# Kernel optimization log

Hardware: AMD Instinct MI355X
Metric: run time of the kernel (lower is better)

## Reference

```python
import jax, jax.numpy as jnp
import numpy as np
import math

B, C, H, W = 8, 512, 32, 32
ENC = 1024
L2 = 64
NH = 8
GROUPS = 32
EPS = 1e-5

def group_norm(x, gamma, beta):
    # x: (B, C, L) GroupNorm with 32 groups (float32)
    b, c, l = x.shape
    xg = x.reshape(b, GROUPS, (c // GROUPS) * l)
    mean = xg.mean(-1, keepdims=True)
    var = xg.var(-1, keepdims=True)
    xn = ((xg - mean) * jax.lax.rsqrt(var + EPS)).reshape(b, c, l)
    return xn * gamma[None, :, None] + beta[None, :, None]

def conv1x1(w, bias, x):
    # conv_nd(1, in, out, 1): w (out, in), x (B, in, L) -> (B, out, L)
    return jnp.einsum('oc,bcl->bol', w, x) + bias[None, :, None]

def setup_inputs() -> dict:
    key = jax.random.key(0)
    ks = jax.random.split(key, 16)
    s = lambda fan_in: 1.0 / math.sqrt(fan_in)
    inp = {
        'x': jax.random.normal(ks[0], (B, C, H, W), jnp.float32),
        'xf_out': jax.random.normal(ks[1], (B, ENC, L2), jnp.float32),
        'obj_class_embedding': jax.random.normal(ks[2], (B, ENC, L2), jnp.float32),
        'obj_bbox_embedding': jax.random.normal(ks[3], (B, ENC, L2), jnp.float32),
        'image_patch_bbox_embedding': jax.random.normal(ks[4], (B, ENC, H * W), jnp.float32),
        'key_padding_mask': jax.random.bernoulli(ks[5], 0.3, (B, L2)),
        'qkv_w': jax.random.normal(ks[6], (3 * C, C), jnp.float32) * s(C),
        'qkv_b': jnp.zeros((3 * C,), jnp.float32),
        'g_qkv': jnp.ones((C,), jnp.float32),
        'b_qkv': jnp.zeros((C,), jnp.float32),
        'lc_w': jax.random.normal(ks[7], (2 * C, ENC), jnp.float32) * s(ENC),
        'lc_b': jnp.zeros((2 * C,), jnp.float32),
        'lp_w': jax.random.normal(ks[8], (C, ENC), jnp.float32) * s(ENC),
        'lp_b': jnp.zeros((C,), jnp.float32),
        'g_obj': jnp.ones((ENC,), jnp.float32),
        'b_obj': jnp.zeros((ENC,), jnp.float32),
        'g_lpos': jnp.ones((C,), jnp.float32),
        'b_lpos': jnp.zeros((C,), jnp.float32),
        'g_ipos': jnp.ones((C,), jnp.float32),
        'b_ipos': jnp.zeros((C,), jnp.float32),
        # proj_out is zero-initialized in the original (zero_module); use random
        # weights so the projection math is exercised non-trivially.
        'proj_w': jax.random.normal(ks[9], (C, C), jnp.float32) * s(C),
        'proj_b': jnp.zeros((C,), jnp.float32),
    }
    return inp

def reference(x, xf_out, obj_class_embedding, obj_bbox_embedding,
              image_patch_bbox_embedding, key_padding_mask,
              qkv_w, qkv_b, g_qkv, b_qkv, lc_w, lc_b, lp_w, lp_b,
              g_obj, b_obj, g_lpos, b_lpos, g_ipos, b_ipos, proj_w, proj_b):
    b, c, h, w = x.shape
    L1 = h * w
    d = C // NH
    xf = x.reshape(b, c, L1)

    qkv = conv1x1(qkv_w, qkv_b, group_norm(xf, g_qkv, b_qkv))  # (B, 3C, L1)
    q, k, v = jnp.split(qkv, 3, axis=1)
    q = q.reshape(b * NH, d, L1)
    k = k.reshape(b * NH, d, L1)
    v = v.reshape(b * NH, d, L1)

    ipp = group_norm(conv1x1(lp_w, lp_b, image_patch_bbox_embedding), g_ipos, b_ipos)
    ipp = ipp.reshape(b * NH, d, L1)

    q_img = jnp.concatenate([q, ipp], axis=1)  # (B*H, 2d, L1)
    k_img = jnp.concatenate([k, ipp], axis=1)

    lpe = group_norm(conv1x1(lp_w, lp_b, obj_bbox_embedding), g_lpos, b_lpos)
    lpe = lpe.reshape(b * NH, d, L2)

    lce = (xf_out + group_norm(obj_class_embedding, g_obj, b_obj)) / 2
    kl, vl = jnp.split(conv1x1(lc_w, lc_b, lce), 2, axis=1)
    kl = kl.reshape(b * NH, d, L2)
    vl = vl.reshape(b * NH, d, L2)
    k_layout = jnp.concatenate([kl, lpe], axis=1)  # (B*H, 2d, L2)

    k_mix = jnp.concatenate([k_img, k_layout], axis=2)  # (B*H, 2d, L1+L2)
    v_mix = jnp.concatenate([v, vl], axis=2)             # (B*H, d, L1+L2)

    mask = jnp.concatenate([jnp.zeros((b, L1), bool), key_padding_mask], axis=1)  # (B, L1+L2)

    scale = 1.0 / math.sqrt(math.sqrt(2 * C // NH))
    attn = jnp.einsum('bct,bcs->bts', q_img * scale, k_mix * scale)  # (B*H, L1, L1+L2)
    attn = attn.reshape(b, NH, L1, L1 + L2)
    attn = jnp.where(mask[:, None, None, :], -jnp.inf, attn)
    attn = jax.nn.softmax(attn.astype(jnp.float32), axis=-1).astype(attn.dtype)
    attn = attn.reshape(b * NH, L1, L1 + L2)

    out = jnp.einsum('bts,bcs->bct', attn, v_mix).reshape(b, C, L1)
    hproj = conv1x1(proj_w, proj_b, out)
    return (xf + hproj).reshape(b, c, h, w)
```

## Files before the change

kernel.cpp:

```cpp
#include <hip/hip_runtime.h>
#include <math.h>

#define NB 8
#define NC 512
#define NL1 1024
#define NL2 64
#define NLKV 1088
#define NENC 1024
#define EPSV 1e-5f
#define SCALE2 0.08838834764831845f
#define SCALE2Q 0.12752425f
#define DEFER_THR 11.5415603f

typedef _Float16 half8 __attribute__((ext_vector_type(8)));
typedef _Float16 half4 __attribute__((ext_vector_type(4)));
typedef __fp16 fp16x2 __attribute__((ext_vector_type(2)));
typedef float f32x4 __attribute__((ext_vector_type(4)));
typedef float f32x16 __attribute__((ext_vector_type(16)));
typedef unsigned int uint32x2 __attribute__((ext_vector_type(2)));

__device__ __forceinline__ void gload16(const _Float16* g, _Float16* l) {
  __builtin_amdgcn_global_load_lds(
      (const __attribute__((address_space(1))) void*)g,
      (__attribute__((address_space(3))) void*)l, 16, 0, 0);
}

__device__ __forceinline__ unsigned int pkrtz(float a, float b) {
  union { fp16x2 hh; unsigned int uu; } cv;
  cv.hh = __builtin_amdgcn_cvt_pkrtz(a, b);
  return cv.uu;
}

__device__ __forceinline__ float fast_exp2(float x) {
  return __builtin_amdgcn_exp2f(x);
}

__global__ __launch_bounds__(256) void k_init(
    const float* __restrict__ x, const float* __restrict__ obj,
    float* __restrict__ xm, float* __restrict__ xr,
    float* __restrict__ om, float* __restrict__ orr,
    const float* __restrict__ qkv_w, _Float16* __restrict__ w16qkv,
    const float* __restrict__ lp_w, _Float16* __restrict__ w16lp,
    const float* __restrict__ proj_w, _Float16* __restrict__ w16proj,
    const float* __restrict__ lc_w, _Float16* __restrict__ w16lc)
{
  int bid = blockIdx.x;
  if (bid < 512) {
    const float* p; float* meanp; float* rstdp; int n4, n, bg;
    if (bid < 256) {
      bg = bid;
      int b = bg >> 5, g = bg & 31;
      p = x + ((size_t)b * 512 + (size_t)g * 16) * 1024;
      n = 16 * 1024; meanp = xm; rstdp = xr;
    } else {
      bg = bid - 256;
      int b = bg >> 5, g = bg & 31;
      p = obj + ((size_t)b * 1024 + (size_t)g * 32) * 64;
      n = 32 * 64; meanp = om; rstdp = orr;
    }
    n4 = n >> 2;
    float s = 0.f, s2 = 0.f;
    for (int i = threadIdx.x; i < n4; i += 256) {
      float4 v = ((const float4*)p)[i];
      s += v.x + v.y + v.z + v.w;
      s2 += v.x * v.x + v.y * v.y + v.z * v.z + v.w * v.w;
    }
    #pragma unroll
    for (int o = 32; o > 0; o >>= 1) { s += __shfl_down(s, o); s2 += __shfl_down(s2, o); }
    __shared__ float rs[4], rq[4];
    int lane = threadIdx.x & 63, w = threadIdx.x >> 6;
    if (lane == 0) { rs[w] = s; rq[w] = s2; }
    __syncthreads();
    if (threadIdx.x == 0) {
      float S = rs[0] + rs[1] + rs[2] + rs[3];
      float Q = rq[0] + rq[1] + rq[2] + rq[3];
      float m = S / n;
      float v = Q / n - m * m;
      if (v < 0.f) v = 0.f;
      meanp[bg] = m;
      rstdp[bg] = rsqrtf(v + EPSV);
    }
  } else {
    int cb = bid - 512;
    const float* s; _Float16* d; int i4;
    if (cb < 768)        { s = qkv_w;  d = w16qkv;  i4 = cb * 256 + threadIdx.x; }
    else if (cb < 1280)  { s = lp_w;   d = w16lp;   i4 = (cb - 768) * 256 + threadIdx.x; }
    else if (cb < 1536)  { s = proj_w; d = w16proj; i4 = (cb - 1280) * 256 + threadIdx.x; }
    else                 { s = lc_w;   d = w16lc;   i4 = (cb - 1536) * 256 + threadIdx.x; }
    float4 v = *(const float4*)&s[(size_t)i4 * 4];
    half4 o; o.x = (_Float16)v.x; o.y = (_Float16)v.y; o.z = (_Float16)v.z; o.w = (_Float16)v.w;
    *(half4*)&d[(size_t)i4 * 4] = o;
  }
}

__global__ __launch_bounds__(256) void k_prep(
    const float* __restrict__ x, const float* __restrict__ xm, const float* __restrict__ xr,
    const float* __restrict__ g_qkv, const float* __restrict__ b_qkv, _Float16* __restrict__ xT,
    const float* __restrict__ ipbe, _Float16* __restrict__ ipbeT,
    const float* __restrict__ xf_out, const float* __restrict__ obj_class,
    const float* __restrict__ obj_bbox,
    const float* __restrict__ om, const float* __restrict__ orr,
    const float* __restrict__ g_obj, const float* __restrict__ b_obj,
    _Float16* __restrict__ lceT, _Float16* __restrict__ objT)
{
  __shared__ _Float16 tile[64][72];
  const int bid = blockIdx.x;
  const int tl = threadIdx.x & 63;
  if (bid < 1024) {
    const int tt = bid & 15, ct = (bid >> 4) & 7, b = bid >> 7;
    const int c0 = ct * 64, t0 = tt * 64;
    const int cp = threadIdx.x >> 6;
    #pragma unroll
    for (int i = 0; i < 16; i++) {
      int c = c0 + i * 4 + cp;
      float v = x[((size_t)b * NC + c) * NL1 + t0 + tl];
      int g = c >> 4;
      float ga = g_qkv[c] * xr[b * 32 + g];
      float be = b_qkv[c] - xm[b * 32 + g] * ga;
      tile[tl][i * 4 + cp] = (_Float16)(v * ga + be);
    }
    __syncthreads();
    int tr = threadIdx.x >> 2, c16 = (threadIdx.x & 3) * 16;
    _Float16* dst = xT + ((size_t)b * 1024 + t0 + tr) * 512 + c0 + c16;
    *(half8*)dst = *(half8*)&tile[tr][c16];
    *(half8*)(dst + 8) = *(half8*)&tile[tr][c16 + 8];
  } else if (bid < 3072) {
    const int e2 = bid - 1024;
    const int tt = e2 & 15, et = (e2 >> 4) & 15, b = e2 >> 8;
    const int e0 = et * 64, t0 = tt * 64;
    const int ep = threadIdx.x >> 6;
    #pragma unroll
    for (int i = 0; i < 16; i++) {
      int e = e0 + i * 4 + ep;
      tile[tl][i * 4 + ep] = (_Float16)ipbe[((size_t)b * 1024 + e) * 1024 + t0 + tl];
    }
    __syncthreads();
    int tr = threadIdx.x >> 2, c16 = (threadIdx.x & 3) * 16;
    _Float16* d = ipbeT + ((size_t)b * 1024 + t0 + tr) * 1024 + e0 + c16;
    *(half8*)d = *(half8*)&tile[tr][c16];
    *(half8*)(d + 8) = *(half8*)&tile[tr][c16 + 8];
  } else {
    const int e2 = bid - 3072;
    const int et = e2 & 15, which = (e2 >> 4) & 1, b = e2 >> 5;
    const int e0 = et * 64;
    const int ep = threadIdx.x >> 6;
    if (which == 0) {
      #pragma unroll
      for (int i = 0; i < 16; i++) {
        int e = e0 + i * 4 + ep;
        size_t idx = ((size_t)b * 1024 + e) * 64 + tl;
        int g = e >> 5;
        float xn = (obj_class[idx] - om[b * 32 + g]) * orr[b * 32 + g] * g_obj[e] + b_obj[e];
        tile[tl][i * 4 + ep] = (_Float16)(0.5f * (xf_out[idx] + xn));
      }
    } else {
      #pragma unroll
      for (int i = 0; i < 16; i++) {
        int e = e0 + i * 4 + ep;
        tile[tl][i * 4 + ep] = (_Float16)obj_bbox[((size_t)b * 1024 + e) * 64 + tl];
      }
    }
    __syncthreads();
    int tr = threadIdx.x >> 2, c16 = (threadIdx.x & 3) * 16;
    _Float16* dst = (which == 0 ? lceT : objT) + ((size_t)b * 64 + tr) * 1024 + e0 + c16;
    *(half8*)dst = *(half8*)&tile[tr][c16];
    *(half8*)(dst + 8) = *(half8*)&tile[tr][c16 + 8];
  }
}

#define MFMA_CORE(KTOT)                                                                  \
  f32x4 acc[4][4];                                                                       \
  _Pragma("unroll") for (int i_ = 0; i_ < 4; i_++)                                       \
      _Pragma("unroll") for (int j_ = 0; j_ < 4; j_++) acc[i_][j_] = (f32x4)0.f;         \
  {                                                                                      \
    const int rsub = lane >> 3, csrc = (lane & 7) ^ rsub;                                \
    const int NT_ = (KTOT) / 64;                                                         \
    _Pragma("unroll") for (int i = 0; i < 4; i++) {                                      \
      int seg = w * 4 + i;                                                               \
      int row = seg * 8 + rsub;                                                          \
      gload16(Abase + (size_t)(m0 + row) * (KTOT) + csrc * 8, ldsA + seg * 512);         \
      gload16(Bbase + (size_t)(n0 + row) * (KTOT) + csrc * 8, ldsB + seg * 512);         \
    }                                                                                    \
    __syncthreads();                                                                     \
    int cur_ = 0;                                                                        \
    for (int t_ = 0; t_ < NT_; t_++) {                                                   \
      if (t_ + 1 < NT_) {                                                                \
        _Float16* da_ = ldsA + ((cur_ ^ 1) << 13);                                       \
        _Float16* db_ = ldsB + ((cur_ ^ 1) << 13);                                       \
        int kt = (t_ + 1) * 64;                                                          \
        _Pragma("unroll") for (int i = 0; i < 4; i++) {                                  \
          int seg = w * 4 + i;                                                           \
          int row = seg * 8 + rsub;                                                      \
          gload16(Abase + (size_t)(m0 + row) * (KTOT) + kt + csrc * 8, da_ + seg * 512); \
          gload16(Bbase + (size_t)(n0 + row) * (KTOT) + kt + csrc * 8, db_ + seg * 512); \
        }                                                                                \
      }                                                                                  \
      const char* ra_ = (const char*)(ldsA + (cur_ << 13));                              \
      const char* rb_ = (const char*)(ldsB + (cur_ << 13));                              \
      _Pragma("unroll") for (int kk = 0; kk < 2; kk++) {                                 \
        half8 af[4], bf[4];                                                              \
        _Pragma("unroll") for (int mb = 0; mb < 4; mb++) {                               \
          int row = wm + mb * 16 + l15;                                                  \
          af[mb] = *(const half8*)(ra_ + row * 128 +                                     \
                                   ((kk * 64 + lg * 16) ^ ((row & 7) << 4)));            \
        }                                                                                \
        _Pragma("unroll") for (int nb = 0; nb < 4; nb++) {                               \
          int row = wn + nb * 16 + l15;                                                  \
          bf[nb] = *(const half8*)(rb_ + row * 128 +                                     \
                                   ((kk * 64 + lg * 16) ^ ((row & 7) << 4)));            \
        }                                                                                \
        _Pragma("unroll") for (int mb = 0; mb < 4; mb++)                                 \
            _Pragma("unroll") for (int nb = 0; nb < 4; nb++)                             \
                acc[mb][nb] = __builtin_amdgcn_mfma_f32_16x16x32_f16(af[mb], bf[nb],     \
                                                                    acc[mb][nb], 0, 0, 0);\
      }                                                                                  \
      __syncthreads();                                                                   \
      cur_ ^= 1;                                                                         \
    }                                                                                    \
  }

#define MFMA_CORE_N64(KTOT)                                                              \
  f32x4 acc[4][2];                                                                       \
  _Pragma("unroll") for (int i_ = 0; i_ < 4; i_++)                                       \
      _Pragma("unroll") for (int j_ = 0; j_ < 2; j_++) acc[i_][j_] = (f32x4)0.f;         \
  {                                                                                      \
    const int rsub = lane >> 3, csrc = (lane & 7) ^ rsub;                                \
    const int NT_ = (KTOT) / 64;                                                         \
    _Pragma("unroll") for (int i = 0; i < 4; i++) {                                      \
      int seg = w * 4 + i;                                                               \
      int row = seg * 8 + rsub;                                                          \
      gload16(Abase + (size_t)(m0 + row) * (KTOT) + csrc * 8, ldsA + seg * 512);         \
    }                                                                                    \
    _Pragma("unroll") for (int i = 0; i < 2; i++) {                                      \
      int seg = w * 2 + i;                                                               \
      int row = seg * 8 + rsub;                                                          \
      gload16(Bbase + (size_t)row * (KTOT) + csrc * 8, ldsB + seg * 512);                \
    }                                                                                    \
    __syncthreads();                                                                     \
    int cur_ = 0;                                                                        \
    for (int t_ = 0; t_ < NT_; t_++) {                                                   \
      if (t_ + 1 < NT_) {                                                                \
        _Float16* da_ = ldsA + ((cur_ ^ 1) << 13);                                       \
        _Float16* db_ = ldsB + ((cur_ ^ 1) << 12);                                       \
        int kt = (t_ + 1) * 64;                                                          \
        _Pragma("unroll") for (int i = 0; i < 4; i++) {                                  \
          int seg = w * 4 + i;                                                           \
          int row = seg * 8 + rsub;                                                      \
          gload16(Abase + (size_t)(m0 + row) * (KTOT) + kt + csrc * 8, da_ + seg * 512); \
        }                                                                                \
        _Pragma("unroll") for (int i = 0; i < 2; i++) {                                  \
          int seg = w * 2 + i;                                                           \
          int row = seg * 8 + rsub;                                                      \
          gload16(Bbase + (size_t)row * (KTOT) + kt + csrc * 8, db_ + seg * 512);        \
        }                                                                                \
      }                                                                                  \
      const char* ra_ = (const char*)(ldsA + (cur_ << 13));                              \
      const char* rb_ = (const char*)(ldsB + (cur_ << 12));                              \
      _Pragma("unroll") for (int kk = 0; kk < 2; kk++) {                                 \
        half8 af[4], bf[2];                                                              \
        _Pragma("unroll") for (int mb = 0; mb < 4; mb++) {                               \
          int row = wm + mb * 16 + l15;                                                  \
          af[mb] = *(const half8*)(ra_ + row * 128 +                                     \
                                   ((kk * 64 + lg * 16) ^ ((row & 7) << 4)));            \
        }                                                                                \
        _Pragma("unroll") for (int nb = 0; nb < 2; nb++) {                               \
          int row = wn + nb * 16 + l15;                                                  \
          bf[nb] = *(const half8*)(rb_ + row * 128 +                                     \
                                   ((kk * 64 + lg * 16) ^ ((row & 7) << 4)));            \
        }                                                                                \
        _Pragma("unroll") for (int mb = 0; mb < 4; mb++)                                 \
            _Pragma("unroll") for (int nb = 0; nb < 2; nb++)                             \
                acc[mb][nb] = __builtin_amdgcn_mfma_f32_16x16x32_f16(af[mb], bf[nb],     \
                                                                    acc[mb][nb], 0, 0, 0);\
      }                                                                                  \
      __syncthreads();                                                                   \
      cur_ ^= 1;                                                                         \
    }                                                                                    \
  }

__global__ __launch_bounds__(256) void k_mfma_big(
    const _Float16* __restrict__ w16qkv, const float* __restrict__ qkv_b,
    const _Float16* __restrict__ xhatT,
    const _Float16* __restrict__ w16lp, const float* __restrict__ lp_b,
    const _Float16* __restrict__ ipbeT,
    const _Float16* __restrict__ w16lc, const float* __restrict__ lc_b,
    const _Float16* __restrict__ lceT, const _Float16* __restrict__ objT,
    const float* __restrict__ g_lpos, const float* __restrict__ b_lpos,
    _Float16* __restrict__ qT, _Float16* __restrict__ kT, _Float16* __restrict__ vT,
    _Float16* __restrict__ ipp16)
{
  __shared__ _Float16 smem[32768];
  const int bid0 = blockIdx.x;
  const int tid = threadIdx.x, lane = tid & 63, w = tid >> 6;
  const int l15 = lane & 15, lg = lane >> 4;

  if (bid0 < 256) {
    const int nt = bid0 & 7, mt = (bid0 >> 3) & 3, b = bid0 >> 5;
    const int m0 = mt * 128, n0 = nt * 128;
    _Float16* ldsA = smem;
    _Float16* ldsB = smem + 16384;
    const _Float16* Abase = w16lp;
    const _Float16* Bbase = ipbeT + (size_t)b * 1024 * 1024;
    const int wm = (w >> 1) * 64, wn = (w & 1) * 64;
    MFMA_CORE(1024)
    #pragma unroll
    for (int mb = 0; mb < 4; mb++) {
      #pragma unroll
      for (int r = 0; r < 4; r++) {
        int m = m0 + wm + mb * 16 + lg * 4 + r;
        float bia = lp_b[m];
        #pragma unroll
        for (int nb = 0; nb < 4; nb++) {
          int t = n0 + wn + nb * 16 + l15;
          ipp16[((size_t)b * NC + m) * NL1 + t] = (_Float16)(acc[mb][nb][r] + bia);
        }
      }
    }
  } else if (bid0 < 352) {
    const int local = bid0 - 256;
    const int mt = local % 12, b = local / 12;
    const bool islc = (mt < 8);
    const int m0 = (islc ? mt : mt - 8) * 128;
    _Float16* ldsA = smem;
    _Float16* ldsB = smem + 16384;
    float (*red_s)[4] = (float(*)[4])(smem + 24576);
    float (*red_q)[4] = (float(*)[4])(smem + 24608);
    const _Float16* Abase = islc ? w16lc : w16lp;
    const float* bias = islc ? lc_b : lp_b;
    const _Float16* Bbase = (islc ? lceT : objT) + (size_t)b * 64 * 1024;
    const int wm = (w >> 1) * 64, wn = (w & 1) * 32;
    MFMA_CORE_N64(1024)

    if (islc) {
      #pragma unroll
      for (int mb = 0; mb < 4; mb++) {
        #pragma unroll
        for (int r = 0; r < 4; r++) {
          int m = m0 + wm + mb * 16 + lg * 4 + r;
          float bia = bias[m];
          #pragma unroll
          for (int nb = 0; nb < 2; nb++) {
            int l = wn + nb * 16 + l15;
            float val = acc[mb][nb][r] + bia;
            if (m < 512) {
              int h = m >> 6, dc = m & 63;
              kT[(((size_t)b * 8 + h) * 1088 + 1024 + l) * 128 + dc] = (_Float16)val;
            } else {
              int mv = m - 512, h = mv >> 6, dc = mv & 63;
              vT[(((size_t)b * 8 + h) * 64 + dc) * 1088 + 1024 + l] = (_Float16)val;
            }
          }
        }
      }
    } else {
      float vals[4][2][4];
      float ps[4], pq[4];
      #pragma unroll
      for (int mb = 0; mb < 4; mb++) {
        ps[mb] = 0.f; pq[mb] = 0.f;
        #pragma unroll
        for (int r = 0; r < 4; r++) {
          int m = m0 + wm + mb * 16 + lg * 4 + r;
          float bia = bias[m];
          #pragma unroll
          for (int nb = 0; nb < 2; nb++) {
            float val = acc[mb][nb][r] + bia;
            vals[mb][nb][r] = val;
            ps[mb] += val; pq[mb] += val * val;
          }
        }
      }
      #pragma unroll
      for (int mb = 0; mb < 4; mb++) {
        #pragma unroll
        for (int o = 32; o > 0; o >>= 1) {
          ps[mb] += __shfl_xor(ps[mb], o);
          pq[mb] += __shfl_xor(pq[mb], o);
        }
      }
      if (lane == 0) {
        #pragma unroll
        for (int mb = 0; mb < 4; mb++) { red_s[w][mb] = ps[mb]; red_q[w][mb] = pq[mb]; }
      }
      __syncthreads();
      const int wbase = (wm >> 6) * 2;
      #pragma unroll
      for (int mb = 0; mb < 4; mb++) {
        float S = red_s[wbase][mb] + red_s[wbase + 1][mb];
        float Q = red_q[wbase][mb] + red_q[wbase + 1][mb];
        float mean = S * (1.f / 1024.f);
        float var = Q * (1.f / 1024.f) - mean * mean;
        if (var < 0.f) var = 0.f;
        float rstd = rsqrtf(var + EPSV);
        #pragma unroll
        for (int r = 0; r < 4; r++) {
          int c = m0 + wm + mb * 16 + lg * 4 + r;
          float ga = g_lpos[c] * rstd;
          float be = b_lpos[c] - mean * ga;
          int hh = c >> 6, dc = c & 63;
          #pragma unroll
          for (int nb = 0; nb < 2; nb++) {
            int l = wn + nb * 16 + l15;
            float xn = vals[mb][nb][r] * ga + be;
            kT[(((size_t)b * 8 + hh) * 1088 + 1024 + l) * 128 + 64 + dc] = (_Float16)xn;
          }
        }
      }
    }
  } else {
    const int bid = bid0 - 352;
    const int nt = bid & 7, tt = bid >> 3;
    const int mt = tt % 12, b = tt / 12;
    const int m0 = mt * 128, n0 = nt * 128;
    _Float16* ldsA = smem;
    _Float16* ldsB = smem + 16384;
    const _Float16* Abase = w16qkv;
    const _Float16* Bbase = xhatT + (size_t)b * 1024 * 512;
    const int wm = (w >> 1) * 64, wn = (w & 1) * 64;
    MFMA_CORE(512)

    char* tb = (char*)smem;
    if (m0 < 1024) {
      const bool isq = (m0 < 512);
      const float qs = isq ? SCALE2Q : 1.f;
      #pragma unroll
      for (int mb = 0; mb < 4; mb++) {
        #pragma unroll
        for (int r = 0; r < 4; r++) {
          int mcol = wm + mb * 16 + lg * 4 + r;
          float bia = qkv_b[m0 + mcol];
          #pragma unroll
          for (int nb = 0; nb < 4; nb++) {
            int trow = wn + nb * 16 + l15;
            float val = (acc[mb][nb][r] + bia) * qs;
            *(_Float16*)(tb + ((trow * 256 + mcol * 2) ^ ((trow & 7) << 4))) = (_Float16)val;
          }
        }
      }
      __syncthreads();
      #pragma unroll
      for (int it = 0; it < 8; it++) {
        int e = it * 256 + tid;
        int trow = e >> 4, seg = e & 15;
        half8 v = *(const half8*)(tb + ((trow * 256 + seg * 16) ^ ((trow & 7) << 4)));
        if (isq) {
          int mq = m0 + seg * 8, hh = mq >> 6, dc = mq & 63;
          *(half8*)(qT + (((size_t)b * 8 + hh) * 1024 + n0 + trow) * 128 + dc) = v;
        } else {
          int mk = m0 - 512 + seg * 8, hh = mk >> 6, dc = mk & 63;
          *(half8*)(kT + (((size_t)b * 8 + hh) * 1088 + n0 + trow) * 128 + dc) = v;
        }
      }
    } else {
      #pragma unroll
      for (int mb = 0; mb < 4; mb++) {
        #pragma unroll
        for (int r = 0; r < 4; r++) {
          int mrow = wm + mb * 16 + lg * 4 + r;
          float bia = qkv_b[m0 + mrow];
          #pragma unroll
          for (int nb = 0; nb < 4; nb++) {
            int tcol = wn + nb * 16 + l15;
            *(_Float16*)(tb + ((mrow * 256 + tcol * 2) ^ ((mrow & 7) << 4))) =
                (_Float16)(acc[mb][nb][r] + bia);
          }
        }
      }
      __syncthreads();
      #pragma unroll
      for (int it = 0; it < 8; it++) {
        int e = it * 256 + tid;
        int mrow = e >> 4, seg = e & 15;
        half8 v = *(const half8*)(tb + ((mrow * 256 + seg * 16) ^ ((mrow & 7) << 4)));
        int mv = m0 - 1024 + mrow, hh = mv >> 6, dc = mv & 63;
        *(half8*)(vT + (((size_t)b * 8 + hh) * 64 + dc) * 1088 + n0 + seg * 8) = v;
      }
    }
  }
}

__global__ __launch_bounds__(256) void k_mfma_proj(
    const _Float16* __restrict__ Abase, const float* __restrict__ bias,
    const _Float16* __restrict__ Ball, const float* __restrict__ xin,
    float* __restrict__ out)
{
  __shared__ _Float16 smem[24576];
  _Float16* ldsA = smem;
  _Float16* ldsB = smem + 16384;
  const int b = blockIdx.z, mt = blockIdx.y, nt = blockIdx.x;
  const int m0 = mt * 128, n0 = nt * 64;
  const _Float16* Bbase = Ball + (size_t)b * 1024 * 512 + (size_t)n0 * 512;
  const int tid = threadIdx.x, lane = tid & 63, w = tid >> 6;
  const int l15 = lane & 15, lg = lane >> 4;
  const int wm = (w >> 1) * 64, wn = (w & 1) * 32;
  MFMA_CORE_N64(512)
  #pragma unroll
  for (int mb = 0; mb < 4; mb++) {
    #pragma unroll
    for (int r = 0; r < 4; r++) {
      int m = m0 + wm + mb * 16 + lg * 4 + r;
      float bia = bias[m];
      #pragma unroll
      for (int nb = 0; nb < 2; nb++) {
        int t = n0 + wn + nb * 16 + l15;
        size_t idx = ((size_t)b * NC + m) * NL1 + t;
        out[idx] = xin[idx] + acc[mb][nb][r] + bia;
      }
    }
  }
}

__global__ __launch_bounds__(256) void k_ipp_fuse(
    const _Float16* __restrict__ raw,
    const float* __restrict__ gm, const float* __restrict__ gb,
    _Float16* __restrict__ qT, _Float16* __restrict__ kT)
{
  const int g = blockIdx.x, b = blockIdx.y;
  const int tid = threadIdx.x;
  const _Float16* p = raw + ((size_t)b * 512 + (size_t)g * 16) * 1024;
  const int t0 = tid * 4;

  float4 v[16];
  float s = 0.f, s2 = 0.f;
  #pragma unroll
  for (int c = 0; c < 16; c++) {
    half4 hv = *(const half4*)&p[(size_t)c * 1024 + t0];
    v[c].x = (float)hv.x; v[c].y = (float)hv.y; v[c].z = (float)hv.z; v[c].w = (float)hv.w;
    s += v[c].x + v[c].y + v[c].z + v[c].w;
    s2 += v[c].x * v[c].x + v[c].y * v[c].y + v[c].z * v[c].z + v[c].w * v[c].w;
  }
  #pragma unroll
  for (int o = 32; o > 0; o >>= 1) { s += __shfl_down(s, o); s2 += __shfl_down(s2, o); }
  __shared__ float rs[4], rq[4], stat[2];
  int lane = tid & 63, w = tid >> 6;
  if (lane == 0) { rs[w] = s; rq[w] = s2; }
  __syncthreads();
  if (tid == 0) {
    float S = rs[0] + rs[1] + rs[2] + rs[3];
    float Q = rq[0] + rq[1] + rq[2] + rq[3];
    float mn = S / 16384.f;
    float var = Q / 16384.f - mn * mn;
    if (var < 0.f) var = 0.f;
    stat[0] = mn; stat[1] = rsqrtf(var + EPSV);
  }
  __syncthreads();
  const float mn = stat[0], rstd = stat[1];

  float ga[16], be[16];
  #pragma unroll
  for (int c = 0; c < 16; c++) {
    ga[c] = gm[g * 16 + c] * rstd;
    be[c] = gb[g * 16 + c] - mn * ga[c];
  }

  const size_t bh = (size_t)b * 8 + (g >> 2);
  const int dcb = (g & 3) * 16;
  #pragma unroll
  for (int j = 0; j < 4; j++) {
    const int t = t0 + j;
    half8 k0, k1, q0, q1;
    #pragma unroll
    for (int c = 0; c < 8; c++) {
      float4 vc = v[c];
      float e = (j == 0) ? vc.x : (j == 1) ? vc.y : (j == 2) ? vc.z : vc.w;
      float xn = e * ga[c] + be[c];
      k0[c] = (_Float16)xn;
      q0[c] = (_Float16)(SCALE2Q * xn);
    }
    #pragma unroll
    for (int c = 8; c < 16; c++) {
      float4 vc = v[c];
      float e = (j == 0) ? vc.x : (j == 1) ? vc.y : (j == 2) ? vc.z : vc.w;
      float xn = e * ga[c] + be[c];
      k1[c - 8] = (_Float16)xn;
      q1[c - 8] = (_Float16)(SCALE2Q * xn);
    }
    _Float16* qd = qT + (bh * 1024 + t) * 128 + 64 + dcb;
    _Float16* kd = kT + (bh * 1088 + t) * 128 + 64 + dcb;
    *(half8*)qd = q0; *(half8*)(qd + 8) = q1;
    *(half8*)kd = k0; *(half8*)(kd + 8) = k1;
  }
}

__global__ __launch_bounds__(256, 2) void k_attn_mfma(
    const _Float16* __restrict__ qT, const _Float16* __restrict__ kT,
    const _Float16* __restrict__ vT, const int* __restrict__ mask,
    _Float16* __restrict__ attnT)
{
  const int x = blockIdx.x & 7;
  const int k = blockIdx.x >> 3;
  const int bh = x + ((k >> 3) << 3);
  const int qt = k & 7;
  const int b = bh >> 3, h = bh & 7;
  const int tid = threadIdx.x;
  const int lane = tid & 63;
  const int w = tid >> 6;
  const int l31 = lane & 31;
  const int hi = lane >> 5;

  __shared__ _Float16 KsB[3 * 64 * 128];
  __shared__ _Float16 VtB[4 * 64 * 64];

  const int q = qt * 128 + w * 32 + l31;

  half8 aq[8];
  {
    const _Float16* qp = qT + ((size_t)bh * 1024 + q) * 128 + hi * 8;
    #pragma unroll
    for (int kst = 0; kst < 8; kst++) aq[kst] = *(const half8*)(qp + kst * 16);
  }

  unsigned int mbits = 0;
  {
    const int* mp = mask + b * 64;
    #pragma unroll
    for (int sb = 0; sb < 2; sb++) {
      #pragma unroll
      for (int reg = 0; reg < 16; reg++) {
        int s = sb * 32 + (reg & 3) + 8 * (reg >> 2) + 4 * hi;
        if (mp[s]) mbits |= 1u << (sb * 16 + reg);
      }
    }
  }

  f32x16 O0 = (f32x16)0.f, O1 = (f32x16)0.f;
  f32x16 scA0 = (f32x16)0.f, scA1 = (f32x16)0.f;
  f32x16 scB0 = (f32x16)0.f, scB1 = (f32x16)0.f;
  float m_run = -INFINITY, l_run = 0.f;

  const int kxor = (l31 & 7) << 4;
  const int ksrow_off = lane >> 4;
  const int kcsrc_base = lane & 15;
  const int vdc_off = lane >> 3;
  const int vcsrc_base = lane & 7;

#define STAGE_KV(T, KD, VD)                                                          \
  {                                                                                  \
    const int s0_ = (T) * 64;                                                        \
    _Pragma("unroll") for (int r = 0; r < 4; r++) {                                  \
      int seg = r * 4 + w;                                                           \
      int srow = seg * 4 + ksrow_off;                                                \
      int csrc = kcsrc_base ^ (srow & 7);                                            \
      gload16(kT + ((size_t)bh * 1088 + s0_ + srow) * 128 + csrc * 8, (KD) + seg * 512); \
    }                                                                                \
    _Pragma("unroll") for (int r = 0; r < 2; r++) {                                  \
      int seg = r * 4 + w;                                                           \
      int dc = seg * 8 + vdc_off;                                                    \
      int csrc = vcsrc_base ^ (dc & 7);                                              \
      gload16(vT + ((size_t)bh * 64 + dc) * 1088 + s0_ + csrc * 8, (VD) + seg * 512);  \
    }                                                                                \
  }

#define XHALF_FMAX(OUTV, INV)                                                        \
  { unsigned int xi_ = __float_as_uint(INV);                                         \
    uint32x2 xr_ = __builtin_amdgcn_permlane32_swap(xi_, xi_, false, false);         \
    OUTV = fmaxf(__uint_as_float(xr_.x), __uint_as_float(xr_.y)); }
#define XHALF_ADD(OUTV, INV)                                                         \
  { unsigned int xi_ = __float_as_uint(INV);                                         \
    uint32x2 xr_ = __builtin_amdgcn_permlane32_swap(xi_, xi_, false, false);         \
    OUTV = __uint_as_float(xr_.x) + __uint_as_float(xr_.y); }

#define ATTN_ITER(C0, C1, P0, P1, T)                                                 \
  {                                                                                  \
    const int T_ = (T);                                                              \
    if (T_ <= 16) {                                                                  \
      if (T_ <= 14) {                                                                \
        _Float16* kd_ = KsB + ((T_ + 2) % 3) * 8192;                                 \
        _Float16* vd_ = VtB + ((T_ + 2) & 3) * 4096;                                 \
        STAGE_KV(T_ + 2, kd_, vd_)                                                   \
      }                                                                              \
      const char* ksb_ = (const char*)(KsB + (T_ % 3) * 8192);                       \
      C0 = (f32x16)0.f; C1 = (f32x16)0.f;                                            \
      __builtin_amdgcn_s_setprio(1);                                                 \
      _Pragma("unroll") for (int kst = 0; kst < 8; kst++) {                          \
        half8 kf0 = *(const half8*)(ksb_ + ((l31 * 256 + kst * 32 + hi * 16) ^ kxor)); \
        half8 kf1 = *(const half8*)(ksb_ + (((32 + l31) * 256 + kst * 32 + hi * 16) ^ kxor)); \
        C0 = __builtin_amdgcn_mfma_f32_32x32x16_f16(kf0, aq[kst], C0, 0, 0, 0);      \
        C1 = __builtin_amdgcn_mfma_f32_32x32x16_f16(kf1, aq[kst], C1, 0, 0, 0);      \
      }                                                                              \
      __builtin_amdgcn_s_setprio(0);                                                 \
    }                                                                                \
    if (T_ >= 1) {                                                                   \
      if (T_ == 17) {                                                                \
        _Pragma("unroll") for (int i = 0; i < 16; i++) {                             \
          if ((mbits >> i) & 1)        P0[i] = -INFINITY;                            \
          if ((mbits >> (16 + i)) & 1) P1[i] = -INFINITY;                            \
        }                                                                            \
      }                                                                              \
      float mx;                                                                      \
      {                                                                              \
        float a0 = fmaxf(fmaxf(P0[0], P0[1]), P0[2]);                                \
        float a1 = fmaxf(fmaxf(P0[3], P0[4]), P0[5]);                                \
        float a2 = fmaxf(fmaxf(P0[6], P0[7]), P0[8]);                                \
        float a3 = fmaxf(fmaxf(P0[9], P0[10]), P0[11]);                              \
        float a4 = fmaxf(fmaxf(P0[12], P0[13]), P0[14]);                             \
        float a5 = fmaxf(fmaxf(P0[15], P1[0]), P1[1]);                               \
        float a6 = fmaxf(fmaxf(P1[2], P1[3]), P1[4]);                                \
        float a7 = fmaxf(fmaxf(P1[5], P1[6]), P1[7]);                                \
        float a8 = fmaxf(fmaxf(P1[8], P1[9]), P1[10]);                               \
        float a9 = fmaxf(fmaxf(P1[11], P1[12]), P1[13]);                             \
        float aa = fmaxf(P1[14], P1[15]);                                            \
        float b0 = fmaxf(fmaxf(a0, a1), a2);                                         \
        float b1 = fmaxf(fmaxf(a3, a4), a5);                                         \
        float b2 = fmaxf(fmaxf(a6, a7), a8);                                         \
        float b3 = fmaxf(a9, aa);                                                    \
        mx = fmaxf(fmaxf(b0, b1), fmaxf(b2, b3));                                    \
      }                                                                              \
      XHALF_FMAX(mx, mx)                                                             \
      if (__all(mx <= m_run + DEFER_THR)) {                                          \
        float sum = 0.f;                                                             \
        _Pragma("unroll") for (int i = 0; i < 16; i++) {                             \
          float p = fast_exp2(P0[i] - m_run); P0[i] = p; sum += p; }                 \
        _Pragma("unroll") for (int i = 0; i < 16; i++) {                             \
          float p = fast_exp2(P1[i] - m_run); P1[i] = p; sum += p; }                 \
        XHALF_ADD(sum, sum)                                                          \
        l_run += sum;                                                                \
      } else {                                                                       \
        float m_new = fmaxf(m_run, mx);                                              \
        float alpha = fast_exp2(m_run - m_new);                                      \
        float sum = 0.f;                                                             \
        _Pragma("unroll") for (int i = 0; i < 16; i++) {                             \
          float p = fast_exp2(P0[i] - m_new); P0[i] = p; sum += p; }                 \
        _Pragma("unroll") for (int i = 0; i < 16; i++) {                             \
          float p = fast_exp2(P1[i] - m_new); P1[i] = p; sum += p; }                 \
        XHALF_ADD(sum, sum)                                                          \
        l_run = l_run * alpha + sum;                                                 \
        m_run = m_new;                                                               \
        _Pragma("unroll") for (int i = 0; i < 16; i++) { O0[i] *= alpha; O1[i] *= alpha; } \
      }                                                                              \
      const char* vtb_ = (const char*)(VtB + ((T_ - 1) & 3) * 4096);                 \
      __builtin_amdgcn_s_setprio(1);                                                 \
      _Pragma("unroll") for (int sb = 0; sb < 2; sb++) {                             \
        _Pragma("unroll") for (int k2 = 0; k2 < 2; k2++) {                           \
          const int kst = sb * 2 + k2;                                               \
          unsigned int pa0, pa1, pb0, pb1;                                           \
          if (sb == 0) {                                                             \
            pa0 = pkrtz(P0[8 * k2 + 0], P0[8 * k2 + 1]);                             \
            pa1 = pkrtz(P0[8 * k2 + 2], P0[8 * k2 + 3]);                             \
            pb0 = pkrtz(P0[8 * k2 + 4], P0[8 * k2 + 5]);                             \
            pb1 = pkrtz(P0[8 * k2 + 6], P0[8 * k2 + 7]);                             \
          } else {                                                                   \
            pa0 = pkrtz(P1[8 * k2 + 0], P1[8 * k2 + 1]);                             \
            pa1 = pkrtz(P1[8 * k2 + 2], P1[8 * k2 + 3]);                             \
            pb0 = pkrtz(P1[8 * k2 + 4], P1[8 * k2 + 5]);                             \
            pb1 = pkrtz(P1[8 * k2 + 6], P1[8 * k2 + 7]);                             \
          }                                                                          \
          uint32x2 r0_ = __builtin_amdgcn_permlane32_swap(pa0, pb0, false, false);   \
          uint32x2 r1_ = __builtin_amdgcn_permlane32_swap(pa1, pb1, false, false);   \
          union { unsigned int u[4]; half8 hh; } pf;                                 \
          pf.u[0] = r0_.x;                                                           \
          pf.u[1] = r1_.x;                                                           \
          pf.u[2] = r0_.y;                                                           \
          pf.u[3] = r1_.y;                                                           \
          half8 vf0 = *(const half8*)(vtb_ + ((l31 * 128 + kst * 32 + hi * 16) ^ kxor)); \
          half8 vf1 = *(const half8*)(vtb_ + (((32 + l31) * 128 + kst * 32 + hi * 16) ^ kxor)); \
          O0 = __builtin_amdgcn_mfma_f32_32x32x16_f16(vf0, pf.hh, O0, 0, 0, 0);      \
          O1 = __builtin_amdgcn_mfma_f32_32x32x16_f16(vf1, pf.hh, O1, 0, 0, 0);      \
        }                                                                            \
      }                                                                              \
      __builtin_amdgcn_s_setprio(0);                                                 \
    }                                                                                \
    if (T_ < 17) {                                                                   \
      if (T_ <= 14)      asm volatile("s_waitcnt vmcnt(8)" ::: "memory");            \
      else if (T_ == 15) asm volatile("s_waitcnt vmcnt(2)" ::: "memory");            \
      else               asm volatile("s_waitcnt vmcnt(0)" ::: "memory");            \
      __builtin_amdgcn_s_barrier();                                                  \
    }                                                                                \
  }

  STAGE_KV(0, KsB, VtB)
  STAGE_KV(1, KsB + 8192, VtB + 4096)
  asm volatile("s_waitcnt vmcnt(8)" ::: "memory");
  __builtin_amdgcn_s_barrier();

  for (int t = 0; t < 18; t += 2) {
    ATTN_ITER(scA0, scA1, scB0, scB1, t)
    ATTN_ITER(scB0, scB1, scA0, scA1, t + 1)
  }

  float inv = 1.f / l_run;
  _Float16* op = attnT + ((size_t)b * 1024 + q) * 512 + h * 64;
  #pragma unroll
  for (int i = 0; i < 16; i += 2) {
    int dc = (i & 3) + 8 * (i >> 2) + 4 * hi;
    unsigned int c0 = pkrtz(O0[i] * inv, O0[i + 1] * inv);
    unsigned int c1 = pkrtz(O1[i] * inv, O1[i + 1] * inv);
    *(unsigned int*)(op + dc) = c0;
    *(unsigned int*)(op + 32 + dc) = c1;
  }
}

extern "C" void kernel_launch(void* const* d_in, const int* in_sizes, int n_in,
                              void* d_out, int out_size, void* d_ws, size_t ws_size,
                              hipStream_t stream) {
  const float* x         = (const float*)d_in[0];
  const float* xf_out    = (const float*)d_in[1];
  const float* obj_class = (const float*)d_in[2];
  const float* obj_bbox  = (const float*)d_in[3];
  const float* ipbe      = (const float*)d_in[4];
  const int*   mask      = (const int*)d_in[5];
  const float* qkv_w     = (const float*)d_in[6];
  const float* qkv_b     = (const float*)d_in[7];
  const float* g_qkv     = (const float*)d_in[8];
  const float* b_qkv     = (const float*)d_in[9];
  const float* lc_w      = (const float*)d_in[10];
  const float* lc_b      = (const float*)d_in[11];
  const float* lp_w      = (const float*)d_in[12];
  const float* lp_b      = (const float*)d_in[13];
  const float* g_obj     = (const float*)d_in[14];
  const float* b_obj     = (const float*)d_in[15];
  const float* g_lpos    = (const float*)d_in[16];
  const float* b_lpos    = (const float*)d_in[17];
  const float* g_ipos    = (const float*)d_in[18];
  const float* b_ipos    = (const float*)d_in[19];
  const float* proj_w    = (const float*)d_in[20];
  const float* proj_b    = (const float*)d_in[21];
  float* out = (float*)d_out;

  _Float16* f16b = (_Float16*)d_ws;
  _Float16* qT      = f16b;
  _Float16* kT      = qT + 8388608;
  _Float16* vT      = kT + 8912896;
  _Float16* xhatT   = vT + 4456448;
  _Float16* ipbeT   = xhatT + 4194304;
  _Float16* attnT   = ipbeT + 8388608;
  _Float16* w16qkv  = attnT + 4194304;
  _Float16* w16lp   = w16qkv + 786432;
  _Float16* w16proj = w16lp + 524288;
  _Float16* w16lc   = w16proj + 262144;
  _Float16* lceT    = w16lc + 1048576;
  _Float16* objT    = lceT + 524288;
  _Float16* ipp16   = objT + 524288;
  float* st = (float*)(ipp16 + 4194304);
  float* xm = st, * xr = st + 256, * om = st + 512, * orr = st + 768;

  dim3 blk(256);
  k_init<<<dim3(3072), blk, 0, stream>>>(x, obj_class, xm, xr, om, orr,
                                         qkv_w, w16qkv, lp_w, w16lp, proj_w, w16proj, lc_w, w16lc);
  k_prep<<<dim3(3328), blk, 0, stream>>>(x, xm, xr, g_qkv, b_qkv, xhatT,
                                         ipbe, ipbeT,
                                         xf_out, obj_class, obj_bbox, om, orr, g_obj, b_obj,
                                         lceT, objT);
  k_mfma_big<<<dim3(1120), blk, 0, stream>>>(w16qkv, qkv_b, xhatT,
                                             w16lp, lp_b, ipbeT,
                                             w16lc, lc_b, lceT, objT,
                                             g_lpos, b_lpos,
                                             qT, kT, vT, ipp16);
  k_ipp_fuse<<<dim3(32, 8), blk, 0, stream>>>(ipp16, g_ipos, b_ipos, qT, kT);
  k_attn_mfma<<<dim3(512), blk, 0, stream>>>(qT, kT, vT, mask, attnT);
  k_mfma_proj<<<dim3(16, 4, 8), blk, 0, stream>>>(w16proj, proj_b, attnT, x, out);
}
```

Measured before the change: 125.0 us.

## Process two query tiles per wave in attention, halving grid and K/V loads

```diff
diff --git a/kernel.cpp b/kernel.cpp
--- a/kernel.cpp
+++ b/kernel.cpp
@@ -582,15 +582,14 @@
   }
 }
 
-__global__ __launch_bounds__(256, 2) void k_attn_mfma(
+__global__ __launch_bounds__(256, 1) void k_attn_mfma(
     const _Float16* __restrict__ qT, const _Float16* __restrict__ kT,
     const _Float16* __restrict__ vT, const int* __restrict__ mask,
     _Float16* __restrict__ attnT)
 {
-  const int x = blockIdx.x & 7;
-  const int k = blockIdx.x >> 3;
-  const int bh = x + ((k >> 3) << 3);
-  const int qt = k & 7;
+  const int bid = blockIdx.x;
+  const int bh = bid >> 2;
+  const int qt = bid & 3;
   const int b = bh >> 3, h = bh & 7;
   const int tid = threadIdx.x;
   const int lane = tid & 63;
@@ -599,15 +598,20 @@
   const int hi = lane >> 5;
 
   __shared__ _Float16 KsB[3 * 64 * 128];
-  __shared__ _Float16 VtB[4 * 64 * 64];
-
-  const int q = qt * 128 + w * 32 + l31;
-
-  half8 aq[8];
+  __shared__ _Float16 VtB[3 * 64 * 64];
+
+  const int qA = qt * 256 + w * 64 + l31;
+  const int qB = qA + 32;
+
+  half8 aqA[8], aqB[8];
   {
-    const _Float16* qp = qT + ((size_t)bh * 1024 + q) * 128 + hi * 8;
-    #pragma unroll
-    for (int kst = 0; kst < 8; kst++) aq[kst] = *(const half8*)(qp + kst * 16);
+    const _Float16* qpA = qT + ((size_t)bh * 1024 + qA) * 128 + hi * 8;
+    const _Float16* qpB = qT + ((size_t)bh * 1024 + qB) * 128 + hi * 8;
+    #pragma unroll
+    for (int kst = 0; kst < 8; kst++) {
+      aqA[kst] = *(const half8*)(qpA + kst * 16);
+      aqB[kst] = *(const half8*)(qpB + kst * 16);
+    }
   }
 
   unsigned int mbits = 0;
@@ -623,10 +627,10 @@
     }
   }
 
-  f32x16 O0 = (f32x16)0.f, O1 = (f32x16)0.f;
-  f32x16 scA0 = (f32x16)0.f, scA1 = (f32x16)0.f;
-  f32x16 scB0 = (f32x16)0.f, scB1 = (f32x16)0.f;
-  float m_run = -INFINITY, l_run = 0.f;
+  f32x16 OA0 = (f32x16)0.f, OA1 = (f32x16)0.f;
+  f32x16 OB0 = (f32x16)0.f, OB1 = (f32x16)0.f;
+  float mA = -INFINITY, lA = 0.f;
+  float mB = -INFINITY, lB = 0.f;
 
   const int kxor = (l31 & 7) << 4;
   const int ksrow_off = lane >> 4;
@@ -660,133 +664,147 @@
     uint32x2 xr_ = __builtin_amdgcn_permlane32_swap(xi_, xi_, false, false);         \
     OUTV = __uint_as_float(xr_.x) + __uint_as_float(xr_.y); }
 
-#define ATTN_ITER(C0, C1, P0, P1, T)                                                 \
+#define SOFTMAX_G(P0, P1, MRUN, LRUN, O0, O1)                                        \
   {                                                                                  \
-    const int T_ = (T);                                                              \
-    if (T_ <= 16) {                                                                  \
-      if (T_ <= 14) {                                                                \
-        _Float16* kd_ = KsB + ((T_ + 2) % 3) * 8192;                                 \
-        _Float16* vd_ = VtB + ((T_ + 2) & 3) * 4096;                                 \
-        STAGE_KV(T_ + 2, kd_, vd_)                                                   \
-      }                                                                              \
-      const char* ksb_ = (const char*)(KsB + (T_ % 3) * 8192);                       \
-      C0 = (f32x16)0.f; C1 = (f32x16)0.f;                                            \
-      __builtin_amdgcn_s_setprio(1);                                                 \
-      _Pragma("unroll") for (int kst = 0; kst < 8; kst++) {                          \
-        half8 kf0 = *(const half8*)(ksb_ + ((l31 * 256 + kst * 32 + hi * 16) ^ kxor)); \
-        half8 kf1 = *(const half8*)(ksb_ + (((32 + l31) * 256 + kst * 32 + hi * 16) ^ kxor)); \
-        C0 = __builtin_amdgcn_mfma_f32_32x32x16_f16(kf0, aq[kst], C0, 0, 0, 0);      \
-        C1 = __builtin_amdgcn_mfma_f32_32x32x16_f16(kf1, aq[kst], C1, 0, 0, 0);      \
-      }                                                                              \
-      __builtin_amdgcn_s_setprio(0);                                                 \
+    float mx;                                                                        \
+    {                                                                                \
+      float a0 = fmaxf(fmaxf(P0[0], P0[1]), P0[2]);                                  \
+      float a1 = fmaxf(fmaxf(P0[3], P0[4]), P0[5]);                                  \
+      float a2 = fmaxf(fmaxf(P0[6], P0[7]), P0[8]);                                  \
+      float a3 = fmaxf(fmaxf(P0[9], P0[10]), P0[11]);                                \
+      float a4 = fmaxf(fmaxf(P0[12], P0[13]), P0[14]);                               \
+      float a5 = fmaxf(fmaxf(P0[15], P1[0]), P1[1]);                                 \
+      float a6 = fmaxf(fmaxf(P1[2], P1[3]), P1[4]);                                  \
+      float a7 = fmaxf(fmaxf(P1[5], P1[6]), P1[7]);                                  \
+      float a8 = fmaxf(fmaxf(P1[8], P1[9]), P1[10]);                                 \
+      float a9 = fmaxf(fmaxf(P1[11], P1[12]), P1[13]);                               \
+      float aa = fmaxf(P1[14], P1[15]);                                              \
+      float b0 = fmaxf(fmaxf(a0, a1), a2);                                           \
+      float b1 = fmaxf(fmaxf(a3, a4), a5);                                           \
+      float b2 = fmaxf(fmaxf(a6, a7), a8);                                           \
+      float b3 = fmaxf(a9, aa);                                                      \
+      mx = fmaxf(fmaxf(b0, b1), fmaxf(b2, b3));                                      \
     }                                                                                \
-    if (T_ >= 1) {                                                                   \
-      if (T_ == 17) {                                                                \
-        _Pragma("unroll") for (int i = 0; i < 16; i++) {                             \
-          if ((mbits >> i) & 1)        P0[i] = -INFINITY;                            \
-          if ((mbits >> (16 + i)) & 1) P1[i] = -INFINITY;                            \
-        }                                                                            \
-      }                                                                              \
-      float mx;                                                                      \
-      {                                                                              \
-        float a0 = fmaxf(fmaxf(P0[0], P0[1]), P0[2]);                                \
-        float a1 = fmaxf(fmaxf(P0[3], P0[4]), P0[5]);                                \
-        float a2 = fmaxf(fmaxf(P0[6], P0[7]), P0[8]);                                \
-        float a3 = fmaxf(fmaxf(P0[9], P0[10]), P0[11]);                              \
-        float a4 = fmaxf(fmaxf(P0[12], P0[13]), P0[14]);                             \
-        float a5 = fmaxf(fmaxf(P0[15], P1[0]), P1[1]);                               \
-        float a6 = fmaxf(fmaxf(P1[2], P1[3]), P1[4]);                                \
-        float a7 = fmaxf(fmaxf(P1[5], P1[6]), P1[7]);                                \
-        float a8 = fmaxf(fmaxf(P1[8], P1[9]), P1[10]);                               \
-        float a9 = fmaxf(fmaxf(P1[11], P1[12]), P1[13]);                             \
-        float aa = fmaxf(P1[14], P1[15]);                                            \
-        float b0 = fmaxf(fmaxf(a0, a1), a2);                                         \
-        float b1 = fmaxf(fmaxf(a3, a4), a5);                                         \
-        float b2 = fmaxf(fmaxf(a6, a7), a8);                                         \
-        float b3 = fmaxf(a9, aa);                                                    \
-        mx = fmaxf(fmaxf(b0, b1), fmaxf(b2, b3));                                    \
-      }                                                                              \
-      XHALF_FMAX(mx, mx)                                                             \
-      if (__all(mx <= m_run + DEFER_THR)) {                                          \
-        float sum = 0.f;                                                             \
-        _Pragma("unroll") for (int i = 0; i < 16; i++) {                             \
-          float p = fast_exp2(P0[i] - m_run); P0[i] = p; sum += p; }                 \
-        _Pragma("unroll") for (int i = 0; i < 16; i++) {                             \
-          float p = fast_exp2(P1[i] - m_run); P1[i] = p; sum += p; }                 \
-        XHALF_ADD(sum, sum)                                                          \
-        l_run += sum;                                                                \
-      } else {                                                                       \
-        float m_new = fmaxf(m_run, mx);                                              \
-        float alpha = fast_exp2(m_run - m_new);                                      \
-        float sum = 0.f;                                                             \
-        _Pragma("unroll") for (int i = 0; i < 16; i++) {                             \
-          float p = fast_exp2(P0[i] - m_new); P0[i] = p; sum += p; }                 \
-        _Pragma("unroll") for (int i = 0; i < 16; i++) {                             \
-          float p = fast_exp2(P1[i] - m_new); P1[i] = p; sum += p; }                 \
-        XHALF_ADD(sum, sum)                                                          \
-        l_run = l_run * alpha + sum;                                                 \
-        m_run = m_new;                                                               \
-        _Pragma("unroll") for (int i = 0; i < 16; i++) { O0[i] *= alpha; O1[i] *= alpha; } \
-      }                                                                              \
-      const char* vtb_ = (const char*)(VtB + ((T_ - 1) & 3) * 4096);                 \
-      __builtin_amdgcn_s_setprio(1);                                                 \
-      _Pragma("unroll") for (int sb = 0; sb < 2; sb++) {                             \
-        _Pragma("unroll") for (int k2 = 0; k2 < 2; k2++) {                           \
-          const int kst = sb * 2 + k2;                                               \
-          unsigned int pa0, pa1, pb0, pb1;                                           \
-          if (sb == 0) {                                                             \
-            pa0 = pkrtz(P0[8 * k2 + 0], P0[8 * k2 + 1]);                             \
-            pa1 = pkrtz(P0[8 * k2 + 2], P0[8 * k2 + 3]);                             \
-            pb0 = pkrtz(P0[8 * k2 + 4], P0[8 * k2 + 5]);                             \
-            pb1 = pkrtz(P0[8 * k2 + 6], P0[8 * k2 + 7]);                             \
-          } else {                                                                   \
-            pa0 = pkrtz(P1[8 * k2 + 0], P1[8 * k2 + 1]);                             \
-            pa1 = pkrtz(P1[8 * k2 + 2], P1[8 * k2 + 3]);                             \
-            pb0 = pkrtz(P1[8 * k2 + 4], P1[8 * k2 + 5]);                             \
-            pb1 = pkrtz(P1[8 * k2 + 6], P1[8 * k2 + 7]);                             \
-          }                                                                          \
-          uint32x2 r0_ = __builtin_amdgcn_permlane32_swap(pa0, pb0, false, false);   \
-          uint32x2 r1_ = __builtin_amdgcn_permlane32_swap(pa1, pb1, false, false);   \
-          union { unsigned int u[4]; half8 hh; } pf;                                 \
-          pf.u[0] = r0_.x;                                                           \
-          pf.u[1] = r1_.x;                                                           \
-          pf.u[2] = r0_.y;                                                           \
-          pf.u[3] = r1_.y;                                                           \
-          half8 vf0 = *(const half8*)(vtb_ + ((l31 * 128 + kst * 32 + hi * 16) ^ kxor)); \
-          half8 vf1 = *(const half8*)(vtb_ + (((32 + l31) * 128 + kst * 32 + hi * 16) ^ kxor)); \
-          O0 = __builtin_amdgcn_mfma_f32_32x32x16_f16(vf0, pf.hh, O0, 0, 0, 0);      \
-          O1 = __builtin_amdgcn_mfma_f32_32x32x16_f16(vf1, pf.hh, O1, 0, 0, 0);      \
-        }                                                                            \
-      }                                                                              \
-      __builtin_amdgcn_s_setprio(0);                                                 \
+    XHALF_FMAX(mx, mx)                                                               \
+    if (__all(mx <= MRUN + DEFER_THR)) {                                             \
+      float sum = 0.f;                                                               \
+      _Pragma("unroll") for (int i = 0; i < 16; i++) {                               \
+        float p = fast_exp2(P0[i] - MRUN); P0[i] = p; sum += p; }                    \
+      _Pragma("unroll") for (int i = 0; i < 16; i++) {                               \
+        float p = fast_exp2(P1[i] - MRUN); P1[i] = p; sum += p; }                    \
+      XHALF_ADD(sum, sum)                                                            \
+      LRUN += sum;                                                                   \
+    } else {                                                                         \
+      float m_new = fmaxf(MRUN, mx);                                                 \
+      float alpha = fast_exp2(MRUN - m_new);                                         \
+      float sum = 0.f;                                                               \
+      _Pragma("unroll") for (int i = 0; i < 16; i++) {                               \
+        float p = fast_exp2(P0[i] - m_new); P0[i] = p; sum += p; }                   \
+      _Pragma("unroll") for (int i = 0; i < 16; i++) {                               \
+        float p = fast_exp2(P1[i] - m_new); P1[i] = p; sum += p; }                   \
+      XHALF_ADD(sum, sum)                                                            \
+      LRUN = LRUN * alpha + sum;                                                     \
+      MRUN = m_new;                                                                  \
+      _Pragma("unroll") for (int i = 0; i < 16; i++) { O0[i] *= alpha; O1[i] *= alpha; } \
     }                                                                                \
-    if (T_ < 17) {                                                                   \
-      if (T_ <= 14)      asm volatile("s_waitcnt vmcnt(8)" ::: "memory");            \
-      else if (T_ == 15) asm volatile("s_waitcnt vmcnt(2)" ::: "memory");            \
-      else               asm volatile("s_waitcnt vmcnt(0)" ::: "memory");            \
-      __builtin_amdgcn_s_barrier();                                                  \
+  }
+
+#define PACK_PF(PFU, P0, P1)                                                         \
+  { unsigned int pa0, pa1, pb0, pb1;                                                 \
+    if (sb == 0) {                                                                   \
+      pa0 = pkrtz(P0[8 * k2 + 0], P0[8 * k2 + 1]);                                   \
+      pa1 = pkrtz(P0[8 * k2 + 2], P0[8 * k2 + 3]);                                   \
+      pb0 = pkrtz(P0[8 * k2 + 4], P0[8 * k2 + 5]);                                   \
+      pb1 = pkrtz(P0[8 * k2 + 6], P0[8 * k2 + 7]);                                   \
+    } else {                                                                         \
+      pa0 = pkrtz(P1[8 * k2 + 0], P1[8 * k2 + 1]);                                   \
+      pa1 = pkrtz(P1[8 * k2 + 2], P1[8 * k2 + 3]);                                   \
+      pb0 = pkrtz(P1[8 * k2 + 4], P1[8 * k2 + 5]);                                   \
+      pb1 = pkrtz(P1[8 * k2 + 6], P1[8 * k2 + 7]);                                   \
     }                                                                                \
-  }
+    uint32x2 r0_ = __builtin_amdgcn_permlane32_swap(pa0, pb0, false, false);         \
+    uint32x2 r1_ = __builtin_amdgcn_permlane32_swap(pa1, pb1, false, false);         \
+    PFU.u[0] = r0_.x; PFU.u[1] = r1_.x; PFU.u[2] = r0_.y; PFU.u[3] = r1_.y; }
 
   STAGE_KV(0, KsB, VtB)
   STAGE_KV(1, KsB + 8192, VtB + 4096)
-  asm volatile("s_waitcnt vmcnt(8)" ::: "memory");
+  asm volatile("s_waitcnt vmcnt(6)" ::: "memory");
   __builtin_amdgcn_s_barrier();
 
-  for (int t = 0; t < 18; t += 2) {
-    ATTN_ITER(scA0, scA1, scB0, scB1, t)
-    ATTN_ITER(scB0, scB1, scA0, scA1, t + 1)
-  }
-
-  float inv = 1.f / l_run;
-  _Float16* op = attnT + ((size_t)b * 1024 + q) * 512 + h * 64;
+  int bufR = 0;
+  for (int t = 0; t <= 16; t++) {
+    int bufS = bufR + 2; if (bufS >= 3) bufS -= 3;
+    if (t <= 14) {
+      _Float16* kd_ = KsB + bufS * 8192;
+      _Float16* vd_ = VtB + bufS * 4096;
+      STAGE_KV(t + 2, kd_, vd_)
+    }
+    const char* ksb_ = (const char*)(KsB + bufR * 8192);
+
+    f32x16 scA0 = (f32x16)0.f, scA1 = (f32x16)0.f;
+    f32x16 scB0 = (f32x16)0.f, scB1 = (f32x16)0.f;
+    __builtin_amdgcn_s_setprio(1);
+    #pragma unroll
+    for (int kst = 0; kst < 8; kst++) {
+      half8 kf0 = *(const half8*)(ksb_ + ((l31 * 256 + kst * 32 + hi * 16) ^ kxor));
+      half8 kf1 = *(const half8*)(ksb_ + (((32 + l31) * 256 + kst * 32 + hi * 16) ^ kxor));
+      scA0 = __builtin_amdgcn_mfma_f32_32x32x16_f16(kf0, aqA[kst], scA0, 0, 0, 0);
+      scA1 = __builtin_amdgcn_mfma_f32_32x32x16_f16(kf1, aqA[kst], scA1, 0, 0, 0);
+      scB0 = __builtin_amdgcn_mfma_f32_32x32x16_f16(kf0, aqB[kst], scB0, 0, 0, 0);
+      scB1 = __builtin_amdgcn_mfma_f32_32x32x16_f16(kf1, aqB[kst], scB1, 0, 0, 0);
+    }
+    __builtin_amdgcn_s_setprio(0);
+
+    if (t == 16) {
+      #pragma unroll
+      for (int i = 0; i < 16; i++) {
+        if ((mbits >> i) & 1)        { scA0[i] = -INFINITY; scB0[i] = -INFINITY; }
+        if ((mbits >> (16 + i)) & 1) { scA1[i] = -INFINITY; scB1[i] = -INFINITY; }
+      }
+    }
+
+    SOFTMAX_G(scA0, scA1, mA, lA, OA0, OA1)
+    SOFTMAX_G(scB0, scB1, mB, lB, OB0, OB1)
+
+    const char* vtb_ = (const char*)(VtB + bufR * 4096);
+    __builtin_amdgcn_s_setprio(1);
+    #pragma unroll
+    for (int sb = 0; sb < 2; sb++) {
+      #pragma unroll
+      for (int k2 = 0; k2 < 2; k2++) {
+        const int kst = sb * 2 + k2;
+        union { unsigned int u[4]; half8 hh; } pfA, pfB;
+        PACK_PF(pfA, scA0, scA1)
+        PACK_PF(pfB, scB0, scB1)
+        half8 vf0 = *(const half8*)(vtb_ + ((l31 * 128 + kst * 32 + hi * 16) ^ kxor));
+        half8 vf1 = *(const half8*)(vtb_ + (((32 + l31) * 128 + kst * 32 + hi * 16) ^ kxor));
+        OA0 = __builtin_amdgcn_mfma_f32_32x32x16_f16(vf0, pfA.hh, OA0, 0, 0, 0);
+        OA1 = __builtin_amdgcn_mfma_f32_32x32x16_f16(vf1, pfA.hh, OA1, 0, 0, 0);
+        OB0 = __builtin_amdgcn_mfma_f32_32x32x16_f16(vf0, pfB.hh, OB0, 0, 0, 0);
+        OB1 = __builtin_amdgcn_mfma_f32_32x32x16_f16(vf1, pfB.hh, OB1, 0, 0, 0);
+      }
+    }
+    __builtin_amdgcn_s_setprio(0);
+
+    if (t < 16) {
+      if (t <= 14) asm volatile("s_waitcnt vmcnt(6)" ::: "memory");
+      else         asm volatile("s_waitcnt vmcnt(0)" ::: "memory");
+      __builtin_amdgcn_s_barrier();
+    }
+    bufR = bufR + 1; if (bufR >= 3) bufR -= 3;
+  }
+
+  float invA = 1.f / lA;
+  float invB = 1.f / lB;
+  _Float16* opA = attnT + ((size_t)b * 1024 + qA) * 512 + h * 64;
+  _Float16* opB = attnT + ((size_t)b * 1024 + qB) * 512 + h * 64;
   #pragma unroll
   for (int i = 0; i < 16; i += 2) {
     int dc = (i & 3) + 8 * (i >> 2) + 4 * hi;
-    unsigned int c0 = pkrtz(O0[i] * inv, O0[i + 1] * inv);
-    unsigned int c1 = pkrtz(O1[i] * inv, O1[i + 1] * inv);
-    *(unsigned int*)(op + dc) = c0;
-    *(unsigned int*)(op + 32 + dc) = c1;
+    *(unsigned int*)(opA + dc)      = pkrtz(OA0[i] * invA, OA0[i + 1] * invA);
+    *(unsigned int*)(opA + 32 + dc) = pkrtz(OA1[i] * invA, OA1[i + 1] * invA);
+    *(unsigned int*)(opB + dc)      = pkrtz(OB0[i] * invB, OB0[i + 1] * invB);
+    *(unsigned int*)(opB + 32 + dc) = pkrtz(OB1[i] * invB, OB1[i + 1] * invB);
   }
 }
 
@@ -847,6 +865,6 @@
                                              g_lpos, b_lpos,
                                              qT, kT, vT, ipp16);
   k_ipp_fuse<<<dim3(32, 8), blk, 0, stream>>>(ipp16, g_ipos, b_ipos, qT, kT);
-  k_attn_mfma<<<dim3(512), blk, 0, stream>>>(qT, kT, vT, mask, attnT);
+  k_attn_mfma<<<dim3(256), blk, 0, stream>>>(qT, kT, vT, mask, attnT);
   k_mfma_proj<<<dim3(16, 4, 8), blk, 0, stream>>>(w16proj, proj_b, attnT, x, out);
 }
```

Result: slower. 137.9 us (+10.3%).
